# Performance work log

Measured on AMD Instinct MI355X. Metric: run time of the kernel, lower is better.

Reference implementation:

```python
import jax, jax.numpy as jnp
import numpy as np

B, T, C = 2, 4096, 768
H = 12
D = C // H  # head_dim = 64


def setup_inputs() -> dict:
    key = jax.random.key(0)
    k1, k2, k3 = jax.random.split(key, 3)
    x = jax.random.normal(k1, (B, T, C), dtype=jnp.float32)
    Wqkv = jax.random.normal(k2, (C, 3 * C), dtype=jnp.float32) * (C ** -0.5)
    Wproj = jax.random.normal(k3, (C, C), dtype=jnp.float32) * (C ** -0.5)
    bproj = jnp.zeros((C,), dtype=jnp.float32)
    return {"x": x, "Wqkv": Wqkv, "Wproj": Wproj, "bproj": bproj}


def reference(x, Wqkv, Wproj, bproj):
    b, t, c = x.shape
    # qkv projection (no bias), split into heads: [3, B, H, T, D]
    qkv = (x @ Wqkv).reshape(b, t, 3, H, D).transpose(2, 0, 3, 1, 4)
    q, k, v = qkv[0], qkv[1], qkv[2]
    scale = D ** -0.5
    # full causal score matrix [B, H, T, T] (faithful to naive impl)
    scores = jnp.einsum('bhqd,bhkd->bhqk', q, k) * scale
    causal = jnp.tril(jnp.ones((t, t), dtype=bool))
    scores = jnp.where(causal[None, None], scores, -jnp.inf)
    attn = jax.nn.softmax(scores, axis=-1)
    out = jnp.einsum('bhqk,bhkd->bhqd', attn, v)
    out = out.transpose(0, 2, 1, 3).reshape(b, t, c)
    return out @ Wproj + bproj
```

## Files before the change

### kernel.cpp

```cpp
#include <hip/hip_runtime.h>

#define B_ 2
#define T_ 4096
#define C_ 768
#define H_ 12
#define D_ 64
#define NTASK 768

typedef __attribute__((ext_vector_type(8))) short bf16x8;
typedef __attribute__((ext_vector_type(4))) float f32x4;
typedef __attribute__((ext_vector_type(16))) float f32x16;

__device__ __forceinline__ unsigned short f2bf(float f) {
  union { float f; unsigned u; } v; v.f = f;
  unsigned r = v.u + 0x7fffu + ((v.u >> 16) & 1u);
  return (unsigned short)(r >> 16);
}

__device__ __forceinline__ float exp2_hw(float x) {
  float r;
  asm("v_exp_f32 %0, %1" : "=v"(r) : "v"(x));
  return r;
}

__device__ __forceinline__ void gll16(const void* g, void* l) {
  __builtin_amdgcn_global_load_lds((const __attribute__((address_space(1))) void*)g,
                                   (__attribute__((address_space(3))) void*)l, 16, 0, 0);
}


__global__ __launch_bounds__(256) void cast_bf16_k(const float* __restrict__ in,
                                                   unsigned short* __restrict__ out, int n4) {
  int i = blockIdx.x * 256 + threadIdx.x;
  if (i >= n4) return;
  float4 v = ((const float4*)in)[i];
  union { unsigned short s[4]; unsigned long long u; } o;
  o.s[0] = f2bf(v.x); o.s[1] = f2bf(v.y); o.s[2] = f2bf(v.z); o.s[3] = f2bf(v.w);
  ((unsigned long long*)out)[i] = o.u;
}

__global__ __launch_bounds__(256) void tcast_bf16_k(const float* __restrict__ in,
                                                    unsigned short* __restrict__ out,
                                                    int R, int C, unsigned* cnt) {
  int idx = blockIdx.x * 256 + threadIdx.x;
  if (cnt != nullptr && idx == 0) *cnt = 0u;
  if (idx >= R * C) return;
  int r = idx / C, c = idx - r * C;
  out[(size_t)c * R + r] = f2bf(in[idx]);
}


#define QSCALE 0.1803368801111243f

template <int MODE>
__global__ __launch_bounds__(256) void gemm_k(const unsigned short* __restrict__ A,
                                              const unsigned short* __restrict__ Bt,
                                              int K,
                                              unsigned short* __restrict__ q_out,
                                              unsigned short* __restrict__ k_out,
                                              unsigned short* __restrict__ vt_out,
                                              float* __restrict__ f_out,
                                              const float* __restrict__ bias) {
  __shared__ short a_lds[128 * 32];
  __shared__ short b_lds[128 * 32];
  const int tid = threadIdx.x;
  const int wave = tid >> 6, lane = tid & 63;
  const int wm = wave >> 1, wn = wave & 1;
  const int lr = lane & 15, lc = lane >> 4;
  const int m0 = blockIdx.x * 128, n0 = blockIdx.y * 128;

  f32x4 acc[4][4];
  for (int mi = 0; mi < 4; ++mi)
    for (int ni = 0; ni < 4; ++ni) acc[mi][ni] = (f32x4){0.f, 0.f, 0.f, 0.f};

  for (int k0 = 0; k0 < K; k0 += 32) {
    __syncthreads();
    for (int p = 0; p < 2; ++p) {
      int chunk = p * 256 + wave * 64 + lane;
      int r = chunk >> 2, cc = chunk & 3;
      int c = cc ^ ((r >> 1) & 3);
      int base = (p * 256 + wave * 64) * 8;
      gll16(A + (size_t)(m0 + r) * K + k0 + c * 8, a_lds + base);
      gll16(Bt + (size_t)(n0 + r) * K + k0 + c * 8, b_lds + base);
    }
    __syncthreads();
    bf16x8 af[4], bfrag[4];
    for (int mi = 0; mi < 4; ++mi) {
      int r = wm * 64 + mi * 16 + lr;
      af[mi] = *(const bf16x8*)&a_lds[r * 32 + (lc ^ ((r >> 1) & 3)) * 8];
    }
    for (int ni = 0; ni < 4; ++ni) {
      int r = wn * 64 + ni * 16 + lr;
      bfrag[ni] = *(const bf16x8*)&b_lds[r * 32 + (lc ^ ((r >> 1) & 3)) * 8];
    }
    for (int mi = 0; mi < 4; ++mi)
      for (int ni = 0; ni < 4; ++ni)
        acc[mi][ni] = __builtin_amdgcn_mfma_f32_16x16x32_bf16(af[mi], bfrag[ni], acc[mi][ni], 0, 0, 0);
  }

  if (MODE == 0) {
    for (int mi = 0; mi < 4; ++mi)
      for (int ni = 0; ni < 4; ++ni) {
        int nn = n0 + wn * 64 + ni * 16 + lr;
        int which = nn / 768;
        int rem = nn - which * 768;
        int h = rem >> 6, d = rem & 63;
        for (int r = 0; r < 4; ++r) {
          int m = m0 + wm * 64 + mi * 16 + lc * 4 + r;
          int b = m >> 12, t = m & (T_ - 1);
          float av = acc[mi][ni][r];
          if (which == 0) av *= QSCALE;
          unsigned short val = f2bf(av);
          size_t bh = (size_t)(b * H_ + h);
          if (which == 0)      q_out[(bh * T_ + t) * D_ + d] = val;
          else if (which == 1) k_out[(bh * T_ + t) * D_ + d] = val;
          else                 vt_out[(bh * D_ + d) * T_ + t] = val;
        }
      }
  } else {
    for (int mi = 0; mi < 4; ++mi)
      for (int ni = 0; ni < 4; ++ni) {
        int nn = n0 + wn * 64 + ni * 16 + lr;
        float bv = bias[nn];
        for (int r = 0; r < 4; ++r) {
          int m = m0 + wm * 64 + mi * 16 + lc * 4 + r;
          f_out[(size_t)m * C_ + nn] = acc[mi][ni][r] + bv;
        }
      }
  }
}


#define PACK8(SV, O)                                                              \
  do {                                                                            \
    unsigned w0, w1, w2, w3, w4, w5, w6, w7;                                      \
    asm("v_cvt_pk_bf16_f32 %0, %1, %2" : "=v"(w0) : "v"(SV[0]), "v"(SV[1]));      \
    asm("v_cvt_pk_bf16_f32 %0, %1, %2" : "=v"(w1) : "v"(SV[2]), "v"(SV[3]));      \
    asm("v_cvt_pk_bf16_f32 %0, %1, %2" : "=v"(w2) : "v"(SV[4]), "v"(SV[5]));      \
    asm("v_cvt_pk_bf16_f32 %0, %1, %2" : "=v"(w3) : "v"(SV[6]), "v"(SV[7]));      \
    asm("v_cvt_pk_bf16_f32 %0, %1, %2" : "=v"(w4) : "v"(SV[8]), "v"(SV[9]));      \
    asm("v_cvt_pk_bf16_f32 %0, %1, %2" : "=v"(w5) : "v"(SV[10]), "v"(SV[11]));    \
    asm("v_cvt_pk_bf16_f32 %0, %1, %2" : "=v"(w6) : "v"(SV[12]), "v"(SV[13]));    \
    asm("v_cvt_pk_bf16_f32 %0, %1, %2" : "=v"(w7) : "v"(SV[14]), "v"(SV[15]));    \
    asm("v_permlane32_swap_b32 %0, %1" : "+v"(w0), "+v"(w2));                     \
    asm("v_permlane32_swap_b32 %0, %1" : "+v"(w1), "+v"(w3));                     \
    asm("v_permlane32_swap_b32 %0, %1" : "+v"(w4), "+v"(w6));                     \
    asm("v_permlane32_swap_b32 %0, %1" : "+v"(w5), "+v"(w7));                     \
    pw[(O) + 0] = w0; pw[(O) + 1] = w1; pw[(O) + 2] = w2; pw[(O) + 3] = w3;       \
    pw[(O) + 4] = w4; pw[(O) + 5] = w5; pw[(O) + 6] = w6; pw[(O) + 7] = w7;       \
  } while (0)

__global__ __launch_bounds__(256) void flash3_k(const unsigned short* __restrict__ Qg,
                                                const unsigned short* __restrict__ Kg,
                                                const unsigned short* __restrict__ Vtg,
                                                unsigned short* __restrict__ Og,
                                                unsigned* __restrict__ cnt) {
  __shared__ short k_lds[2][8 * 512];
  __shared__ short vt_lds[2][8 * 512];
  __shared__ int task_s;

  const int tid = threadIdx.x;
  const int wave = tid >> 6, lane = tid & 63;
  const int lq = lane & 31;

  for (;;) {
    if (tid == 0) task_s = (int)atomicAdd(cnt, 1u);
    __syncthreads();
    const int task = task_s;
    if (task >= NTASK) return;

    const int qi = 31 - (task / 24);
    const int bh = task - (task / 24) * 24;
    const int q0 = qi * 128;
    const int qw = q0 + wave * 32;
    const int q_g = qw + lq;

    const size_t kbase = (size_t)bh * T_ * D_;
    const size_t vbase = (size_t)bh * D_ * T_;

    const unsigned short* qrow = Qg + kbase + (size_t)q_g * D_;
    bf16x8 qf[4];
#pragma unroll
    for (int t = 0; t < 4; ++t) qf[t] = *(const bf16x8*)(qrow + t * 16 + (lane >> 5) * 8);

    f32x16 accT0, accT1;
#pragma unroll
    for (int r = 0; r < 16; ++r) { accT0[r] = 0.f; accT1[r] = 0.f; }
    float m = -INFINITY, l = 0.f;

    const int nt = 2 * qi + 2;

    auto stage = [&](int it, int buf) {
      const int kv = it * 64;
#pragma unroll
      for (int p = 0; p < 2; ++p) {
        int f = p * 4 + wave;
        int th = f >> 1, hf = f & 1;
        gll16(Kg + kbase + (size_t)(kv + hf * 32 + lq) * D_ + th * 16 + (lane >> 5) * 8,
              &k_lds[buf][f * 512]);
        gll16(Vtg + vbase + (size_t)(hf * 32 + lq) * T_ + kv + th * 16 + (lane >> 5) * 8,
              &vt_lds[buf][f * 512]);
      }
    };

    stage(0, 0);
    __syncthreads();

    for (int it = 0; it < nt; ++it) {
      const int kv = it * 64;
      const int buf = it & 1;
      if (it + 1 < nt) stage(it + 1, buf ^ 1);

      if (kv <= qw + 31) {
        f32x16 s0, s1;
#pragma unroll
        for (int r = 0; r < 16; ++r) { s0[r] = 0.f; s1[r] = 0.f; }
        __builtin_amdgcn_s_setprio(1);
#pragma unroll
        for (int t = 0; t < 4; ++t) {
          bf16x8 kf0 = *(const bf16x8*)&k_lds[buf][(t * 2 + 0) * 512 + lane * 8];
          bf16x8 kf1 = *(const bf16x8*)&k_lds[buf][(t * 2 + 1) * 512 + lane * 8];
          s0 = __builtin_amdgcn_mfma_f32_32x32x16_bf16(kf0, qf[t], s0, 0, 0, 0);
          s1 = __builtin_amdgcn_mfma_f32_32x32x16_bf16(kf1, qf[t], s1, 0, 0, 0);
        }
        __builtin_amdgcn_s_setprio(0);

        const int hi = lane >> 5;
        if (kv + 63 > qw) {
#pragma unroll
          for (int r = 0; r < 16; ++r) {
            int key0 = kv + ((r & 3) + 8 * (r >> 2) + 4 * hi);
            if (key0 > q_g) s0[r] = -INFINITY;
            if (key0 + 32 > q_g) s1[r] = -INFINITY;
          }
        }

        float rx = fmaxf(s0[0], s0[1]);
#pragma unroll
        for (int r = 2; r < 16; ++r) rx = fmaxf(rx, s0[r]);
#pragma unroll
        for (int r = 0; r < 16; ++r) rx = fmaxf(rx, s1[r]);
        rx = fmaxf(rx, __shfl_xor(rx, 32));
        if (!__all(rx <= m + 8.f)) {
          float mn = fmaxf(m, rx);
          float al = exp2_hw(m - mn);
          m = mn;
          l *= al;
#pragma unroll
          for (int r = 0; r < 16; ++r) { accT0[r] *= al; accT1[r] *= al; }
        }
        float sum = 0.f;
#pragma unroll
        for (int r = 0; r < 16; ++r) { s0[r] = exp2_hw(s0[r] - m); sum += s0[r]; }
#pragma unroll
        for (int r = 0; r < 16; ++r) { s1[r] = exp2_hw(s1[r] - m); sum += s1[r]; }
        sum += __shfl_xor(sum, 32);
        l += sum;

        unsigned pw[16];
        PACK8(s0, 0);
        PACK8(s1, 8);

        __builtin_amdgcn_s_setprio(1);
#pragma unroll
        for (int ks = 0; ks < 4; ++ks) {
          union { unsigned u[4]; bf16x8 v; } pb;
          pb.u[0] = pw[ks * 4 + 0]; pb.u[1] = pw[ks * 4 + 1];
          pb.u[2] = pw[ks * 4 + 2]; pb.u[3] = pw[ks * 4 + 3];
          bf16x8 vf0 = *(const bf16x8*)&vt_lds[buf][(ks * 2 + 0) * 512 + lane * 8];
          bf16x8 vf1 = *(const bf16x8*)&vt_lds[buf][(ks * 2 + 1) * 512 + lane * 8];
          accT0 = __builtin_amdgcn_mfma_f32_32x32x16_bf16(vf0, pb.v, accT0, 0, 0, 0);
          accT1 = __builtin_amdgcn_mfma_f32_32x32x16_bf16(vf1, pb.v, accT1, 0, 0, 0);
        }
        __builtin_amdgcn_s_setprio(0);
      }
      __syncthreads();
    }

    const float inv = 1.0f / l;
    const int b = bh / H_, h = bh - b * H_;
    const int hi = lane >> 5;
    unsigned short* orow = Og + ((size_t)b * T_ + q_g) * C_ + h * D_;
#pragma unroll
    for (int g = 0; g < 4; ++g) {
      int d0 = 8 * g + 4 * hi;
      unsigned u0 = (unsigned)f2bf(accT0[4 * g + 0] * inv) | ((unsigned)f2bf(accT0[4 * g + 1] * inv) << 16);
      unsigned u1 = (unsigned)f2bf(accT0[4 * g + 2] * inv) | ((unsigned)f2bf(accT0[4 * g + 3] * inv) << 16);
      *(unsigned*)(orow + d0) = u0;
      *(unsigned*)(orow + d0 + 2) = u1;
      unsigned u2 = (unsigned)f2bf(accT1[4 * g + 0] * inv) | ((unsigned)f2bf(accT1[4 * g + 1] * inv) << 16);
      unsigned u3 = (unsigned)f2bf(accT1[4 * g + 2] * inv) | ((unsigned)f2bf(accT1[4 * g + 3] * inv) << 16);
      *(unsigned*)(orow + 32 + d0) = u2;
      *(unsigned*)(orow + 32 + d0 + 2) = u3;
    }
    __syncthreads();
  }
}


extern "C" void kernel_launch(void* const* d_in, const int* in_sizes, int n_in,
                              void* d_out, int out_size, void* d_ws, size_t ws_size,
                              hipStream_t stream) {
  const float* x     = (const float*)d_in[0];
  const float* Wqkv  = (const float*)d_in[1];
  const float* Wproj = (const float*)d_in[2];
  const float* bproj = (const float*)d_in[3];
  float* out = (float*)d_out;

  char* ws = (char*)d_ws;
  unsigned short* xbf   = (unsigned short*)(ws);
  unsigned short* wqkvt = (unsigned short*)(ws + 12582912);
  unsigned short* wprjt = (unsigned short*)(ws + 16121856);
  unsigned short* Qb    = (unsigned short*)(ws + 17301504);
  unsigned short* Kb    = (unsigned short*)(ws + 29884416);
  unsigned short* Vtb   = (unsigned short*)(ws + 42467328);
  unsigned*       cnt   = (unsigned*)(ws + 55050240);

  cast_bf16_k<<<6144, 256, 0, stream>>>(x, xbf, (B_ * T_ * C_) / 4);
  tcast_bf16_k<<<(C_ * 3 * C_) / 256, 256, 0, stream>>>(Wqkv, wqkvt, C_, 3 * C_, cnt);
  tcast_bf16_k<<<(C_ * C_) / 256, 256, 0, stream>>>(Wproj, wprjt, C_, C_, nullptr);

  gemm_k<0><<<dim3((B_ * T_) / 128, (3 * C_) / 128), 256, 0, stream>>>(
      xbf, wqkvt, C_, Qb, Kb, Vtb, nullptr, nullptr);

  flash3_k<<<512, 256, 0, stream>>>(Qb, Kb, Vtb, xbf, cnt);

  gemm_k<1><<<dim3((B_ * T_) / 128, C_ / 128), 256, 0, stream>>>(
      xbf, wprjt, C_, nullptr, nullptr, nullptr, out, bproj);
}
```

Baseline: 232.1 us.

## Shard flash attention task queue per XCD and pipeline KV staging with waitcnt

Splits the single atomic work queue into 8 queues keyed on blockIdx&7, so each XCD handles 3 fixed heads, which is meant to improve L2 locality and reduce atomic contention. The grid grows to 768 blocks. Per-iteration __syncthreads are replaced with raw s_barrier plus explicit vmcnt waits so the next KV tile load overlaps compute. Row max and sum use tree reductions instead of serial chains, and the output is packed with v_cvt_pk_bf16_f32 into 8-byte stores. The result relies on blocks mapping round-robin to XCDs, and the hand-written waitcnt counting risks reading LDS before the data has arrived.

```diff
diff --git a/kernel.cpp b/kernel.cpp
--- a/kernel.cpp
+++ b/kernel.cpp
@@ -6,6 +6,7 @@
 #define H_ 12
 #define D_ 64
 #define NTASK 768
+#define QTASK 96
 
 typedef __attribute__((ext_vector_type(8))) short bf16x8;
 typedef __attribute__((ext_vector_type(4))) float f32x4;
@@ -43,7 +44,7 @@
                                                     unsigned short* __restrict__ out,
                                                     int R, int C, unsigned* cnt) {
   int idx = blockIdx.x * 256 + threadIdx.x;
-  if (cnt != nullptr && idx == 0) *cnt = 0u;
+  if (cnt != nullptr && idx < 128) cnt[idx] = 0u;
   if (idx >= R * C) return;
   int r = idx / C, c = idx - r * C;
   out[(size_t)c * R + r] = f2bf(in[idx]);
@@ -150,7 +151,7 @@
     pw[(O) + 4] = w4; pw[(O) + 5] = w5; pw[(O) + 6] = w6; pw[(O) + 7] = w7;       \
   } while (0)
 
-__global__ __launch_bounds__(256) void flash3_k(const unsigned short* __restrict__ Qg,
+__global__ __launch_bounds__(256) void flash4_k(const unsigned short* __restrict__ Qg,
                                                 const unsigned short* __restrict__ Kg,
                                                 const unsigned short* __restrict__ Vtg,
                                                 unsigned short* __restrict__ Og,
@@ -162,17 +163,18 @@
   const int tid = threadIdx.x;
   const int wave = tid >> 6, lane = tid & 63;
   const int lq = lane & 31;
+  const int xq = blockIdx.x & 7;
+  unsigned* myq = cnt + xq * 16;
 
   for (;;) {
-    if (tid == 0) task_s = (int)atomicAdd(cnt, 1u);
+    if (tid == 0) task_s = (int)atomicAdd(myq, 1u);
     __syncthreads();
     const int task = task_s;
-    if (task >= NTASK) return;
-
-    const int qi = 31 - (task / 24);
-    const int bh = task - (task / 24) * 24;
-    const int q0 = qi * 128;
-    const int qw = q0 + wave * 32;
+    if (task >= QTASK) return;
+
+    const int qi = 31 - task / 3;
+    const int bh = xq * 3 + (task - (task / 3) * 3);
+    const int qw = qi * 128 + wave * 32;
     const int q_g = qw + lq;
 
     const size_t kbase = (size_t)bh * T_ * D_;
@@ -204,12 +206,22 @@
     };
 
     stage(0, 0);
-    __syncthreads();
 
     for (int it = 0; it < nt; ++it) {
       const int kv = it * 64;
       const int buf = it & 1;
-      if (it + 1 < nt) stage(it + 1, buf ^ 1);
+
+      __builtin_amdgcn_s_barrier();
+      __builtin_amdgcn_sched_barrier(0);
+      if (it + 1 < nt) {
+        stage(it + 1, buf ^ 1);
+        asm volatile("s_waitcnt vmcnt(4)" ::: "memory");
+      } else {
+        asm volatile("s_waitcnt vmcnt(0)" ::: "memory");
+      }
+      __builtin_amdgcn_sched_barrier(0);
+      __builtin_amdgcn_s_barrier();
+      __builtin_amdgcn_sched_barrier(0);
 
       if (kv <= qw + 31) {
         f32x16 s0, s1;
@@ -235,12 +247,16 @@
           }
         }
 
-        float rx = fmaxf(s0[0], s0[1]);
-#pragma unroll
-        for (int r = 2; r < 16; ++r) rx = fmaxf(rx, s0[r]);
-#pragma unroll
-        for (int r = 0; r < 16; ++r) rx = fmaxf(rx, s1[r]);
-        rx = fmaxf(rx, __shfl_xor(rx, 32));
+        float mx[16];
+#pragma unroll
+        for (int r = 0; r < 16; ++r) mx[r] = fmaxf(s0[r], s1[r]);
+#pragma unroll
+        for (int st = 8; st >= 1; st >>= 1)
+#pragma unroll
+          for (int r = 0; r < 8; ++r) {
+            if (r < st) mx[r] = fmaxf(mx[r], mx[r + st]);
+          }
+        float rx = fmaxf(mx[0], __shfl_xor(mx[0], 32));
         if (!__all(rx <= m + 8.f)) {
           float mn = fmaxf(m, rx);
           float al = exp2_hw(m - mn);
@@ -249,13 +265,20 @@
 #pragma unroll
           for (int r = 0; r < 16; ++r) { accT0[r] *= al; accT1[r] *= al; }
         }
-        float sum = 0.f;
-#pragma unroll
-        for (int r = 0; r < 16; ++r) { s0[r] = exp2_hw(s0[r] - m); sum += s0[r]; }
-#pragma unroll
-        for (int r = 0; r < 16; ++r) { s1[r] = exp2_hw(s1[r] - m); sum += s1[r]; }
-        sum += __shfl_xor(sum, 32);
-        l += sum;
+#pragma unroll
+        for (int r = 0; r < 16; ++r) s0[r] = exp2_hw(s0[r] - m);
+#pragma unroll
+        for (int r = 0; r < 16; ++r) s1[r] = exp2_hw(s1[r] - m);
+        float sm[16];
+#pragma unroll
+        for (int r = 0; r < 16; ++r) sm[r] = s0[r] + s1[r];
+#pragma unroll
+        for (int st = 8; st >= 1; st >>= 1)
+#pragma unroll
+          for (int r = 0; r < 8; ++r) {
+            if (r < st) sm[r] += sm[r + st];
+          }
+        l += sm[0] + __shfl_xor(sm[0], 32);
 
         unsigned pw[16];
         PACK8(s0, 0);
@@ -274,7 +297,6 @@
         }
         __builtin_amdgcn_s_setprio(0);
       }
-      __syncthreads();
     }
 
     const float inv = 1.0f / l;
@@ -284,14 +306,17 @@
 #pragma unroll
     for (int g = 0; g < 4; ++g) {
       int d0 = 8 * g + 4 * hi;
-      unsigned u0 = (unsigned)f2bf(accT0[4 * g + 0] * inv) | ((unsigned)f2bf(accT0[4 * g + 1] * inv) << 16);
-      unsigned u1 = (unsigned)f2bf(accT0[4 * g + 2] * inv) | ((unsigned)f2bf(accT0[4 * g + 3] * inv) << 16);
-      *(unsigned*)(orow + d0) = u0;
-      *(unsigned*)(orow + d0 + 2) = u1;
-      unsigned u2 = (unsigned)f2bf(accT1[4 * g + 0] * inv) | ((unsigned)f2bf(accT1[4 * g + 1] * inv) << 16);
-      unsigned u3 = (unsigned)f2bf(accT1[4 * g + 2] * inv) | ((unsigned)f2bf(accT1[4 * g + 3] * inv) << 16);
-      *(unsigned*)(orow + 32 + d0) = u2;
-      *(unsigned*)(orow + 32 + d0 + 2) = u3;
+      float a0 = accT0[4 * g + 0] * inv, a1 = accT0[4 * g + 1] * inv;
+      float a2 = accT0[4 * g + 2] * inv, a3 = accT0[4 * g + 3] * inv;
+      float b0 = accT1[4 * g + 0] * inv, b1 = accT1[4 * g + 1] * inv;
+      float b2 = accT1[4 * g + 2] * inv, b3 = accT1[4 * g + 3] * inv;
+      uint2 ua, ub;
+      asm("v_cvt_pk_bf16_f32 %0, %1, %2" : "=v"(ua.x) : "v"(a0), "v"(a1));
+      asm("v_cvt_pk_bf16_f32 %0, %1, %2" : "=v"(ua.y) : "v"(a2), "v"(a3));
+      asm("v_cvt_pk_bf16_f32 %0, %1, %2" : "=v"(ub.x) : "v"(b0), "v"(b1));
+      asm("v_cvt_pk_bf16_f32 %0, %1, %2" : "=v"(ub.y) : "v"(b2), "v"(b3));
+      *(uint2*)(orow + d0) = ua;
+      *(uint2*)(orow + 32 + d0) = ub;
     }
     __syncthreads();
   }
@@ -323,7 +348,7 @@
   gemm_k<0><<<dim3((B_ * T_) / 128, (3 * C_) / 128), 256, 0, stream>>>(
       xbf, wqkvt, C_, Qb, Kb, Vtb, nullptr, nullptr);
 
-  flash3_k<<<512, 256, 0, stream>>>(Qb, Kb, Vtb, xbf, cnt);
+  flash4_k<<<768, 256, 0, stream>>>(Qb, Kb, Vtb, xbf, cnt);
 
   gemm_k<1><<<dim3((B_ * T_) / 128, C_ / 128), 256, 0, stream>>>(
       xbf, wprjt, C_, nullptr, nullptr, nullptr, out, bproj);
```

Measured after the change: 231.3 us. No clear change (-0.3%).
